# Kernel optimization log

Measured on AMD Instinct MI355X. Metric: run time of the kernel, lower is better.

The kernel has to match this reference:

```python
import jax, jax.numpy as jnp
import numpy as np

N_NODES = 100000
N_EDGES = 1600000
N_FEAT = 128
HIDDEN = 128
N_GRAPHS = 64
N_CLASSES = 10
BN_EPS = 1e-5


def setup_inputs() -> dict:
    key = jax.random.key(0)
    ks = jax.random.split(key, 24)
    glorot = lambda k, o, i: jax.random.normal(k, (o, i), jnp.float32) * (1.0 / np.sqrt(i))
    inp = {
        'x': jax.random.normal(ks[0], (N_NODES, N_FEAT), jnp.float32),
        'edge_index': jax.random.randint(ks[1], (2, N_EDGES), 0, N_NODES, jnp.int64),
        'batch': jnp.sort(jax.random.randint(ks[2], (N_NODES,), 0, N_GRAPHS, jnp.int64)),
        # GCNConv(128 -> 128)
        'gcn_w': glorot(ks[3], HIDDEN, N_FEAT),
        'gcn_b': jnp.zeros((HIDDEN,), jnp.float32),
        # SAGEConv layers 1, 2: lin_l (aggregated, with bias) + lin_r (root, no bias)
        'sage1_wl': glorot(ks[4], HIDDEN, HIDDEN),
        'sage1_bl': jnp.zeros((HIDDEN,), jnp.float32),
        'sage1_wr': glorot(ks[5], HIDDEN, HIDDEN),
        'sage2_wl': glorot(ks[6], HIDDEN, HIDDEN),
        'sage2_bl': jnp.zeros((HIDDEN,), jnp.float32),
        'sage2_wr': glorot(ks[7], HIDDEN, HIDDEN),
        # ClassifierBase: 128 -> 200 -> 100 -> 50 -> 10
        'clf_w0': glorot(ks[8], 200, HIDDEN), 'clf_b0': jnp.zeros((200,), jnp.float32),
        'clf_w1': glorot(ks[9], 100, 200), 'clf_b1': jnp.zeros((100,), jnp.float32),
        'clf_w2': glorot(ks[10], 50, 100), 'clf_b2': jnp.zeros((50,), jnp.float32),
        'clf_w3': glorot(ks[11], N_CLASSES, 50), 'clf_b3': jnp.zeros((N_CLASSES,), jnp.float32),
        # BatchNorm1d (eval mode, running_mean=0, running_var=1)
        'bn0_g': jnp.ones((200,), jnp.float32), 'bn0_b': jnp.zeros((200,), jnp.float32),
        'bn1_g': jnp.ones((100,), jnp.float32), 'bn1_b': jnp.zeros((100,), jnp.float32),
        'bn2_g': jnp.ones((50,), jnp.float32), 'bn2_b': jnp.zeros((50,), jnp.float32),
    }
    return inp


def _gcn_conv(x, src, dst, W, b):
    # PyG GCNConv: add self loops, symmetric deg^{-1/2} normalization
    xw = x @ W.T                                                  # [N, H]
    ones = jnp.ones(src.shape[0], xw.dtype)
    deg = jax.ops.segment_sum(ones, dst, num_segments=N_NODES) + 1.0  # self loops
    dinv = jax.lax.rsqrt(deg)
    norm = dinv[src] * dinv[dst]                                  # [E]
    out = jax.ops.segment_sum(xw[src] * norm[:, None], dst, num_segments=N_NODES)
    out = out + xw * (dinv * dinv)[:, None]                       # self-loop term deg^{-1}
    return out + b


def _sage_conv(x, src, dst, Wl, bl, Wr):
    # PyG SAGEConv (mean aggr): lin_l(mean_{j->i} x_j) + lin_r(x_i)
    ones = jnp.ones(src.shape[0], x.dtype)
    cnt = jax.ops.segment_sum(ones, dst, num_segments=N_NODES)
    agg = jax.ops.segment_sum(x[src], dst, num_segments=N_NODES)
    agg = agg / jnp.maximum(cnt, 1.0)[:, None]
    return agg @ Wl.T + bl + x @ Wr.T


def _bn_eval(h, g, b):
    # eval-mode BatchNorm1d with running_mean=0, running_var=1
    return h * (g / np.sqrt(1.0 + BN_EPS)) + b


def reference(x, edge_index, batch, gcn_w, gcn_b,
              sage1_wl, sage1_bl, sage1_wr, sage2_wl, sage2_bl, sage2_wr,
              clf_w0, clf_b0, clf_w1, clf_b1, clf_w2, clf_b2, clf_w3, clf_b3,
              bn0_g, bn0_b, bn1_g, bn1_b, bn2_g, bn2_b):
    src, dst = edge_index[0], edge_index[1]
    h = _gcn_conv(x, src, dst, gcn_w, gcn_b)          # act_func is None -> no activation
    h = _sage_conv(h, src, dst, sage1_wl, sage1_bl, sage1_wr)
    h = _sage_conv(h, src, dst, sage2_wl, sage2_bl, sage2_wr)
    # global mean pool over graphs
    gcnt = jax.ops.segment_sum(jnp.ones(h.shape[0], h.dtype), batch, num_segments=N_GRAPHS)
    g = jax.ops.segment_sum(h, batch, num_segments=N_GRAPHS) / jnp.maximum(gcnt, 1.0)[:, None]
    # ClassifierBase (eval: dropout inactive), tanh activation
    g = jnp.tanh(_bn_eval(g @ clf_w0.T + clf_b0, bn0_g, bn0_b))
    g = jnp.tanh(_bn_eval(g @ clf_w1.T + clf_b1, bn1_g, bn1_b))
    g = jnp.tanh(_bn_eval(g @ clf_w2.T + clf_b2, bn2_g, bn2_b))
    logits = g @ clf_w3.T + clf_b3
    return jax.nn.softmax(logits, axis=1)             # [B, n_classes]
```

## Files before the change

### kernel.cpp

```cpp
#include <hip/hip_runtime.h>

#define N_NODES 100000
#define N_EDGES 1600000
#define NGRAPH 64
#define NBIN 391
#define EPB 2560
#define NBLK 625
#define CAPB 6144
#define CAPP 7168
#define PSPLIT 8

typedef short s8v __attribute__((ext_vector_type(8)));
typedef float f4v __attribute__((ext_vector_type(4)));
typedef float f2v __attribute__((ext_vector_type(2)));

__device__ __forceinline__ float bflo(unsigned u) { return __uint_as_float(u << 16); }
__device__ __forceinline__ float bfhi(unsigned u) { return __uint_as_float(u & 0xffff0000u); }
__device__ __forceinline__ unsigned short f2bf(float f) {
    unsigned u = __float_as_uint(f);
    u += 0x7fffu + ((u >> 16) & 1u);
    return (unsigned short)(u >> 16);
}
__device__ __forceinline__ float bf2f(unsigned short h) { return __uint_as_float(((unsigned)h) << 16); }
__device__ __forceinline__ unsigned pk(float lo, float hi) {
    return (unsigned)f2bf(lo) | ((unsigned)f2bf(hi) << 16);
}
__device__ __forceinline__ float ldv(const void* p, int i, int f32) {
    return f32 ? ((const float*)p)[i] : bf2f(((const unsigned short*)p)[i]);
}
__device__ __forceinline__ f2v up2(unsigned u) {
    f2v t; t.x = bflo(u); t.y = bfhi(u); return t;
}

__global__ __launch_bounds__(256) void k_setup(const unsigned short* __restrict__ x,
                                               const int* __restrict__ ei,
                                               const int* __restrict__ batch,
                                               int* __restrict__ flags,
                                               int* __restrict__ binCur,
                                               int* __restrict__ gstart,
                                               float* __restrict__ pbuf,
                                               const void* b0, const void* bn0g, const void* bn0b,
                                               const void* b1, const void* bn1g, const void* bn1b,
                                               const void* b2, const void* bn2g, const void* bn2b,
                                               const void* b3) {
    __shared__ int cnt[3];
    int tid = threadIdx.x;
    if (tid < 3) cnt[tid] = 0;
    __syncthreads();
    unsigned short h = x[tid * 37];
    int e = (h >> 7) & 0xFF;
    if (e >= 100 && e <= 150) atomicAdd(&cnt[0], 1);
    if (ei[2 * (tid * 5000) + 1] == 0) atomicAdd(&cnt[1], 1);
    if (batch[2 * (tid * 193) + 1] == 0) atomicAdd(&cnt[2], 1);
    __syncthreads();
    int f = (cnt[0] == 256) ? 0 : 1;
    int b64 = (cnt[2] == 256) ? 1 : 0;
    if (tid == 0) {
        flags[0] = f;
        flags[1] = (cnt[1] == 256) ? 1 : 0;
        flags[2] = b64;
    }
    for (int i = tid; i < NBIN; i += 256) binCur[i] = i * CAPB;
    if (tid <= NGRAPH) {
        int g = tid, lo = 0, hi = N_NODES;
        while (lo < hi) {
            int mid = (lo + hi) >> 1;
            int v = b64 ? batch[2 * mid] : batch[mid];
            if (v < g) lo = mid + 1;
            else hi = mid;
        }
        gstart[g] = lo;
    }
    const float invs = rsqrtf(1.0f + 1e-5f);
    if (tid < 200) {
        float a = ldv(bn0g, tid, f) * invs;
        pbuf[tid] = a;
        pbuf[200 + tid] = ldv(b0, tid, f) * a + ldv(bn0b, tid, f);
    }
    if (tid < 100) {
        float a = ldv(bn1g, tid, f) * invs;
        pbuf[400 + tid] = a;
        pbuf[500 + tid] = ldv(b1, tid, f) * a + ldv(bn1b, tid, f);
    }
    if (tid < 50) {
        float a = ldv(bn2g, tid, f) * invs;
        pbuf[600 + tid] = a;
        pbuf[650 + tid] = ldv(b2, tid, f) * a + ldv(bn2b, tid, f);
    }
    if (tid < 10) pbuf[700 + tid] = ldv(b3, tid, f);
}

__global__ __launch_bounds__(256) void k_binfill(const int* __restrict__ ei,
                                                 int* __restrict__ binCur,
                                                 unsigned* __restrict__ staging,
                                                 const int* __restrict__ flags) {
    __shared__ int cnt[NBIN];
    __shared__ int lofs[NBIN];
    __shared__ int curL[NBIN];
    __shared__ int basg[NBIN];
    __shared__ int sA[512], sB[512];
    __shared__ int sbuf[EPB];
    __shared__ int dbuf[EPB];
    __shared__ unsigned ebuf[EPB];
    __shared__ unsigned short bbuf[EPB];
    int tid = threadIdx.x;
    int i64 = flags[1];
    int base = blockIdx.x * EPB;
    for (int i = tid; i < NBIN; i += 256) cnt[i] = 0;
    __syncthreads();
    #pragma unroll
    for (int k = 0; k < EPB / 512; ++k) {
        int e = base + k * 512 + tid * 2;
        int s0, s1, d0, d1;
        if (i64) {
            uint4 vs = *(const uint4*)(ei + 2 * (size_t)e);
            uint4 vd = *(const uint4*)(ei + 2 * (size_t)(N_EDGES + e));
            s0 = (int)vs.x; s1 = (int)vs.z;
            d0 = (int)vd.x; d1 = (int)vd.z;
        } else {
            int2 vs = *(const int2*)(ei + (size_t)e);
            int2 vd = *(const int2*)(ei + (size_t)N_EDGES + e);
            s0 = vs.x; s1 = vs.y;
            d0 = vd.x; d1 = vd.y;
        }
        int l = k * 512 + tid * 2;
        sbuf[l] = s0; sbuf[l + 1] = s1;
        dbuf[l] = d0; dbuf[l + 1] = d1;
        if ((unsigned)d0 < N_NODES) atomicAdd(&cnt[d0 >> 8], 1);
        if ((unsigned)d1 < N_NODES) atomicAdd(&cnt[d1 >> 8], 1);
    }
    __syncthreads();
    for (int k = tid; k < 512; k += 256) sA[k] = (k < NBIN) ? cnt[k] : 0;
    __syncthreads();
    int* src = sA;
    int* dst = sB;
    for (int off = 1; off < 512; off <<= 1) {
        for (int k = tid; k < 512; k += 256)
            dst[k] = src[k] + ((k >= off) ? src[k - off] : 0);
        __syncthreads();
        int* t = src; src = dst; dst = t;
    }
    int totE = src[NBIN - 1];
    for (int i = tid; i < NBIN; i += 256) {
        int excl = src[i] - cnt[i];
        lofs[i] = excl;
        curL[i] = excl;
        basg[i] = cnt[i] ? atomicAdd(&binCur[i], cnt[i]) : 0;
    }
    __syncthreads();
    #pragma unroll
    for (int k = 0; k < EPB / 256; ++k) {
        int l = k * 256 + tid;
        int d = dbuf[l];
        int s = sbuf[l];
        if ((unsigned)d < N_NODES) {
            s = min(max(s, 0), N_NODES - 1);
            int p = atomicAdd(&curL[d >> 8], 1);
            ebuf[p] = ((unsigned)(d & 255) << 20) | (unsigned)s;
            bbuf[p] = (unsigned short)(d >> 8);
        }
    }
    __syncthreads();
    for (int i = tid; i < totE; i += 256) {
        int bb = bbuf[i];
        int p = basg[bb] + (i - lofs[bb]);
        if (p < (bb + 1) * CAPB) staging[p] = ebuf[i];
    }
}

__global__ __launch_bounds__(256) void k_csr(const unsigned* __restrict__ staging,
                                             const int* __restrict__ binCur,
                                             int* __restrict__ rsA, int* __restrict__ reA,
                                             float* __restrict__ dinv,
                                             int* __restrict__ colidx) {
    __shared__ int deg[256];
    __shared__ int s[256];
    __shared__ int cur[256];
    __shared__ int colbuf[CAPP];
    int b = blockIdx.x, tid = threadIdx.x;
    int n0 = b << 8;
    int nend = min(256, N_NODES - n0);
    int runStart = b * CAPB;
    int outStart = b * CAPP;
    int runLen = min(binCur[b] - runStart, CAPB);
    deg[tid] = 0;
    for (int i = tid; i < CAPP; i += 256) colbuf[i] = N_NODES;
    __syncthreads();
    for (int i = tid; i < runLen; i += 256)
        atomicAdd(&deg[staging[runStart + i] >> 20], 1);
    __syncthreads();
    int myDeg = deg[tid];
    int pdeg = (myDeg + 15) & ~15;
    s[tid] = pdeg;
    __syncthreads();
    for (int off = 1; off < 256; off <<= 1) {
        int x2 = (tid >= off) ? s[tid - off] : 0;
        __syncthreads();
        s[tid] += x2;
        __syncthreads();
    }
    int incl = s[tid];
    int lrs = incl - pdeg;
    if (tid < nend) {
        rsA[n0 + tid] = outStart + lrs;
        reA[n0 + tid] = outStart + lrs + myDeg;
        dinv[n0 + tid] = rsqrtf((float)myDeg + 1.0f);
    }
    cur[tid] = lrs;
    __syncthreads();
    for (int i = tid; i < runLen; i += 256) {
        unsigned e = staging[runStart + i];
        int p = atomicAdd(&cur[e >> 20], 1);
        if (p < CAPP) colbuf[p] = (int)(e & 0xFFFFF);
    }
    __syncthreads();
    int ptot = min(s[255], CAPP);
    for (int i = tid; i < ptot; i += 256) colidx[outStart + i] = colbuf[i];
}

__global__ __launch_bounds__(256) void k_prescale(const void* __restrict__ src,
                                                  const float* __restrict__ dinv,
                                                  unsigned* __restrict__ out,
                                                  unsigned* __restrict__ padA,
                                                  const int* __restrict__ flags) {
    int id = blockIdx.x * 256 + threadIdx.x;
    if (id >= (N_NODES + 1) * 64) return;
    int node = id >> 6;
    if (node == N_NODES) {
        out[id] = 0u;
        padA[id] = 0u;
        return;
    }
    float di = dinv[node];
    float lo, hi;
    if (flags[0]) {
        float2 u = ((const float2*)src)[id];
        lo = u.x; hi = u.y;
    } else {
        unsigned u = ((const unsigned*)src)[id];
        lo = bflo(u); hi = bfhi(u);
    }
    out[id] = pk(di * lo, di * hi);
}

__global__ __launch_bounds__(256) void k_agg(const uint4* __restrict__ xs,
                                             const int* __restrict__ rsA,
                                             const int* __restrict__ reA,
                                             const float* __restrict__ dinv,
                                             unsigned* __restrict__ out, int mode,
                                             const int* __restrict__ col) {
    int lane = threadIdx.x & 63;
    int node = blockIdx.x * 4 + (threadIdx.x >> 6);
    int glane = lane & 15, grp = lane >> 4;
    int rs = rsA[node], re = reA[node];
    int deg = re - rs;
    int pend = rs + ((deg + 15) & ~15);
    f2v a0 = {0.f, 0.f}, a1 = {0.f, 0.f}, a2 = {0.f, 0.f}, a3 = {0.f, 0.f};
    uint4 selfu = make_uint4(0u, 0u, 0u, 0u);
    if (mode == 0) selfu = xs[(unsigned)node * 16u + glane];

    for (int base = rs; base < pend; base += 16) {
        int4 c = *(const int4*)(col + base + grp * 4);
        uint4 u0 = xs[(unsigned)c.x * 16u + glane];
        uint4 u1 = xs[(unsigned)c.y * 16u + glane];
        uint4 u2 = xs[(unsigned)c.z * 16u + glane];
        uint4 u3 = xs[(unsigned)c.w * 16u + glane];
        a0 += up2(u0.x); a1 += up2(u0.y); a2 += up2(u0.z); a3 += up2(u0.w);
        a0 += up2(u1.x); a1 += up2(u1.y); a2 += up2(u1.z); a3 += up2(u1.w);
        a0 += up2(u2.x); a1 += up2(u2.y); a2 += up2(u2.z); a3 += up2(u2.w);
        a0 += up2(u3.x); a1 += up2(u3.y); a2 += up2(u3.z); a3 += up2(u3.w);
    }
    float r[8] = {a0.x, a0.y, a1.x, a1.y, a2.x, a2.y, a3.x, a3.y};
    #pragma unroll
    for (int i = 0; i < 8; ++i) {
        float v = r[i];
        v += __shfl_xor(v, 16, 64);
        v += __shfl_xor(v, 32, 64);
        r[i] = v;
    }
    if (mode == 0) {
        float di = dinv[node];
        r[0] = di * (r[0] + bflo(selfu.x)); r[1] = di * (r[1] + bfhi(selfu.x));
        r[2] = di * (r[2] + bflo(selfu.y)); r[3] = di * (r[3] + bfhi(selfu.y));
        r[4] = di * (r[4] + bflo(selfu.z)); r[5] = di * (r[5] + bfhi(selfu.z));
        r[6] = di * (r[6] + bflo(selfu.w)); r[7] = di * (r[7] + bfhi(selfu.w));
    } else {
        float s = 1.0f / fmaxf((float)deg, 1.0f);
        #pragma unroll
        for (int i = 0; i < 8; ++i) r[i] *= s;
    }
    if (grp == 0) {
        uint4 o;
        o.x = pk(r[0], r[1]); o.y = pk(r[2], r[3]);
        o.z = pk(r[4], r[5]); o.w = pk(r[6], r[7]);
        *(uint4*)(out + (size_t)node * 64 + glane * 4) = o;
    }
}

template <int DUAL>
__global__ __launch_bounds__(256) void k_gemm(const unsigned short* A0,
                                              const void* __restrict__ W0,
                                              const unsigned short* __restrict__ A1,
                                              const void* __restrict__ W1,
                                              const void* __restrict__ bias,
                                              unsigned short* out,
                                              const int* __restrict__ flags) {
    __shared__ __align__(16) unsigned short As[64][136];
    __shared__ __align__(16) unsigned short Ws[128][136];
    int f32 = flags[0];
    int tid = threadIdx.x;
    int lane = tid & 63;
    int rowbase = blockIdx.x * 64;
    int lr = lane & 15, q = lane >> 4;
    int m0 = (tid >> 6) * 16;

    f4v acc[8];
    #pragma unroll
    for (int t = 0; t < 8; ++t) acc[t] = (f4v){0.f, 0.f, 0.f, 0.f};

    #pragma unroll
    for (int p = 0; p < (DUAL ? 2 : 1); ++p) {
        const unsigned short* Ap = p ? A1 : A0;
        const void* Wp = p ? W1 : W0;
        if (p) __syncthreads();
        #pragma unroll
        for (int it = 0; it < 4; ++it) {
            int chunk = tid + it * 256;
            int r = chunk >> 4, c8 = (chunk & 15) * 8;
            int grow = rowbase + r;
            uint4 v = make_uint4(0u, 0u, 0u, 0u);
            if (grow < N_NODES) v = *(const uint4*)(Ap + (size_t)grow * 128 + c8);
            *(uint4*)&As[r][c8] = v;
        }
        if (!f32) {
            const unsigned short* Wf = (const unsigned short*)Wp;
            #pragma unroll
            for (int it = 0; it < 8; ++it) {
                int chunk = tid + it * 256;
                int r = chunk >> 4, c8 = (chunk & 15) * 8;
                *(uint4*)&Ws[r][c8] = *(const uint4*)(Wf + r * 128 + c8);
            }
        } else {
            const float* Wf = (const float*)Wp;
            #pragma unroll
            for (int it = 0; it < 16; ++it) {
                int chunk = tid + it * 256;
                int r = chunk >> 5, c4 = (chunk & 31) * 4;
                float4 v = *(const float4*)(Wf + r * 128 + c4);
                unsigned lo = (unsigned)f2bf(v.x) | ((unsigned)f2bf(v.y) << 16);
                unsigned hi = (unsigned)f2bf(v.z) | ((unsigned)f2bf(v.w) << 16);
                *(uint2*)&Ws[r][c4] = make_uint2(lo, hi);
            }
        }
        __syncthreads();
        #pragma unroll
        for (int k = 0; k < 4; ++k) {
            s8v a = *(const s8v*)&As[m0 + lr][k * 32 + q * 8];
            #pragma unroll
            for (int t = 0; t < 8; ++t) {
                s8v b = *(const s8v*)&Ws[t * 16 + lr][k * 32 + q * 8];
                acc[t] = __builtin_amdgcn_mfma_f32_16x16x32_bf16(a, b, acc[t], 0, 0, 0);
            }
        }
    }
    #pragma unroll
    for (int t = 0; t < 8; ++t) {
        int o = t * 16 + lr;
        float bv = ldv(bias, o, f32);
        #pragma unroll
        for (int j = 0; j < 4; ++j) {
            int m = rowbase + m0 + q * 4 + j;
            if (m < N_NODES) out[(size_t)m * 128 + o] = f2bf(acc[t][j] + bv);
        }
    }
}

__global__ __launch_bounds__(256) void k_pool2(const unsigned* __restrict__ h,
                                               const int* __restrict__ gstart,
                                               float* __restrict__ ppool) {
    __shared__ float part[4][128];
    int g = blockIdx.x / PSPLIT, sl = blockIdx.x % PSPLIT;
    int wave = threadIdx.x >> 6, lane = threadIdx.x & 63;
    int s0 = gstart[g], s1 = gstart[g + 1];
    int n = s1 - s0;
    int chunk = (n + PSPLIT - 1) / PSPLIT;
    int r0 = s0 + sl * chunk;
    int r1 = min(r0 + chunk, s1);
    float a0 = 0.f, a1 = 0.f;
    for (int r = r0 + wave; r < r1; r += 4) {
        unsigned u = h[(size_t)r * 64 + lane];
        a0 += bflo(u);
        a1 += bfhi(u);
    }
    part[wave][2 * lane] = a0;
    part[wave][2 * lane + 1] = a1;
    __syncthreads();
    int t = threadIdx.x;
    if (t < 128) {
        float s = part[0][t] + part[1][t] + part[2][t] + part[3][t];
        ppool[(size_t)blockIdx.x * 128 + t] = s;
    }
}

__global__ void k_cvt_w(const void* w0, const void* w1, const void* w2, const void* w3,
                        float* __restrict__ wbuf, const int* __restrict__ flags) {
    int f = flags[0];
    int i = blockIdx.x * 256 + threadIdx.x;
    if (i < 25600) wbuf[i] = ldv(w0, i, f);
    else if (i < 45600) wbuf[i] = ldv(w1, i - 25600, f);
    else if (i < 50600) wbuf[i] = ldv(w2, i - 45600, f);
    else if (i < 51100) wbuf[i] = ldv(w3, i - 50600, f);
}

__global__ __launch_bounds__(256) void k_clf(const float* __restrict__ ppool,
                                             const int* __restrict__ gstart,
                                             const float* __restrict__ wbuf,
                                             const float* __restrict__ pbuf,
                                             void* outv, const int* __restrict__ flags) {
    __shared__ float gin[128];
    __shared__ float ha[200];
    __shared__ float hb[100];
    int b = blockIdx.x, t = threadIdx.x;
    if (t < 128) {
        float s = 0.f;
        #pragma unroll
        for (int k = 0; k < PSPLIT; ++k) s += ppool[(size_t)(b * PSPLIT + k) * 128 + t];
        int cnt = gstart[b + 1] - gstart[b];
        gin[t] = s / fmaxf((float)cnt, 1.0f);
    }
    __syncthreads();
    if (t < 200) {
        const float4* wr = (const float4*)(wbuf + t * 128);
        float s = 0.f;
        #pragma unroll
        for (int k = 0; k < 32; ++k) {
            float4 v = wr[k];
            s += v.x * gin[4 * k] + v.y * gin[4 * k + 1] + v.z * gin[4 * k + 2] + v.w * gin[4 * k + 3];
        }
        ha[t] = tanhf(s * pbuf[t] + pbuf[200 + t]);
    }
    __syncthreads();
    if (t < 100) {
        const float4* wr = (const float4*)(wbuf + 25600 + t * 200);
        float s = 0.f;
        #pragma unroll
        for (int k = 0; k < 50; ++k) {
            float4 v = wr[k];
            s += v.x * ha[4 * k] + v.y * ha[4 * k + 1] + v.z * ha[4 * k + 2] + v.w * ha[4 * k + 3];
        }
        hb[t] = tanhf(s * pbuf[400 + t] + pbuf[500 + t]);
    }
    __syncthreads();
    if (t < 50) {
        const float4* wr = (const float4*)(wbuf + 45600 + t * 100);
        float s = 0.f;
        #pragma unroll
        for (int k = 0; k < 25; ++k) {
            float4 v = wr[k];
            s += v.x * hb[4 * k] + v.y * hb[4 * k + 1] + v.z * hb[4 * k + 2] + v.w * hb[4 * k + 3];
        }
        gin[t] = tanhf(s * pbuf[600 + t] + pbuf[650 + t]);
    }
    __syncthreads();
    if (t == 0) {
        int f = flags[0];
        float lg[10];
        float mx = -1e30f;
        #pragma unroll
        for (int c = 0; c < 10; ++c) {
            const float* wr = wbuf + 50600 + c * 50;
            float s = 0.f;
            for (int k = 0; k < 50; ++k) s += wr[k] * gin[k];
            s += pbuf[700 + c];
            lg[c] = s;
            mx = fmaxf(mx, s);
        }
        float sum = 0.f;
        #pragma unroll
        for (int c = 0; c < 10; ++c) {
            lg[c] = __expf(lg[c] - mx);
            sum += lg[c];
        }
        float inv = 1.0f / sum;
        #pragma unroll
        for (int c = 0; c < 10; ++c) {
            float v = lg[c] * inv;
            if (f) ((float*)outv)[b * 10 + c] = v;
            else ((unsigned short*)outv)[b * 10 + c] = f2bf(v);
        }
    }
}

extern "C" void kernel_launch(void* const* d_in, const int* in_sizes, int n_in,
                              void* d_out, int out_size, void* d_ws, size_t ws_size,
                              hipStream_t stream) {
    const unsigned short* x16 = (const unsigned short*)d_in[0];
    const int* ei = (const int*)d_in[1];
    const int* batch = (const int*)d_in[2];

    char* ws = (char*)d_ws;
    size_t off = 0;
    auto alloc = [&](size_t bytes) {
        size_t r = off;
        off = (off + bytes + 255) & ~(size_t)255;
        return r;
    };
    int* flags = (int*)(ws + alloc(256));
    int* rsA = (int*)(ws + alloc((size_t)N_NODES * 4));
    int* reA = (int*)(ws + alloc((size_t)N_NODES * 4));
    int* colidx = (int*)(ws + alloc((size_t)NBIN * CAPP * 4));
    float* dinv = (float*)(ws + alloc((size_t)N_NODES * 4));
    int* binCur = (int*)(ws + alloc(NBIN * 4));
    int* gstart = (int*)(ws + alloc((NGRAPH + 1) * 4));
    float* pbuf = (float*)(ws + alloc(710 * 4));
    float* ppool = (float*)(ws + alloc((size_t)NGRAPH * PSPLIT * 128 * 4));
    float* wbuf = (float*)(ws + alloc(51100 * 4));
    unsigned short* bufA = (unsigned short*)(ws + alloc((size_t)(N_NODES + 1) * 128 * 2));
    unsigned short* bufB = (unsigned short*)(ws + alloc((size_t)(N_NODES + 1) * 128 * 2));
    unsigned* staging = (unsigned*)bufA;

    k_setup<<<1, 256, 0, stream>>>(x16, ei, batch, flags, binCur, gstart, pbuf,
                                   d_in[12], d_in[19], d_in[20],
                                   d_in[14], d_in[21], d_in[22],
                                   d_in[16], d_in[23], d_in[24], d_in[18]);
    k_cvt_w<<<200, 256, 0, stream>>>(d_in[11], d_in[13], d_in[15], d_in[17], wbuf, flags);

    k_binfill<<<NBLK, 256, 0, stream>>>(ei, binCur, staging, flags);
    k_csr<<<NBIN, 256, 0, stream>>>(staging, binCur, rsA, reA, dinv, colidx);

    k_prescale<<<((N_NODES + 1) * 64 + 255) / 256, 256, 0, stream>>>(
        (const void*)x16, dinv, (unsigned*)bufB, (unsigned*)bufA, flags);
    k_agg<<<N_NODES / 4, 256, 0, stream>>>((const uint4*)bufB, rsA, reA, dinv,
                                           (unsigned*)bufA, 0, colidx);
    k_gemm<0><<<(N_NODES + 63) / 64, 256, 0, stream>>>(bufA, d_in[3], nullptr, nullptr, d_in[4],
                                                       bufA, flags);
    k_agg<<<N_NODES / 4, 256, 0, stream>>>((const uint4*)bufA, rsA, reA, dinv,
                                           (unsigned*)bufB, 1, colidx);
    k_gemm<1><<<(N_NODES + 63) / 64, 256, 0, stream>>>(bufB, d_in[5], bufA, d_in[7], d_in[6],
                                                       bufB, flags);
    k_agg<<<N_NODES / 4, 256, 0, stream>>>((const uint4*)bufB, rsA, reA, dinv,
                                           (unsigned*)bufA, 1, colidx);
    k_gemm<1><<<(N_NODES + 63) / 64, 256, 0, stream>>>(bufA, d_in[8], bufB, d_in[10], d_in[9],
                                                       bufA, flags);
    k_pool2<<<NGRAPH * PSPLIT, 256, 0, stream>>>((const unsigned*)bufA, gstart, ppool);
    k_clf<<<NGRAPH, 256, 0, stream>>>(ppool, gstart, wbuf, pbuf, d_out, flags);
}
```

Before: 500.2 us.

## Fold GCN prescale into aggregation, merge setup kernels, enlarge GEMM tiles

New measurement: 473.2 us. -5.4%, faster.

```diff
diff --git a/kernel.cpp b/kernel.cpp
--- a/kernel.cpp
+++ b/kernel.cpp
@@ -39,28 +39,39 @@
                                                int* __restrict__ binCur,
                                                int* __restrict__ gstart,
                                                float* __restrict__ pbuf,
+                                               float* __restrict__ wbuf,
+                                               const void* w0, const void* w1,
+                                               const void* w2, const void* w3,
                                                const void* b0, const void* bn0g, const void* bn0b,
                                                const void* b1, const void* bn1g, const void* bn1b,
                                                const void* b2, const void* bn2g, const void* bn2b,
                                                const void* b3) {
     __shared__ int cnt[3];
-    int tid = threadIdx.x;
+    int tid = threadIdx.x, bid = blockIdx.x;
     if (tid < 3) cnt[tid] = 0;
     __syncthreads();
     unsigned short h = x[tid * 37];
     int e = (h >> 7) & 0xFF;
     if (e >= 100 && e <= 150) atomicAdd(&cnt[0], 1);
-    if (ei[2 * (tid * 5000) + 1] == 0) atomicAdd(&cnt[1], 1);
-    if (batch[2 * (tid * 193) + 1] == 0) atomicAdd(&cnt[2], 1);
+    if (bid == 0) {
+        if (ei[2 * (tid * 5000) + 1] == 0) atomicAdd(&cnt[1], 1);
+        if (batch[2 * (tid * 193) + 1] == 0) atomicAdd(&cnt[2], 1);
+    }
     __syncthreads();
     int f = (cnt[0] == 256) ? 0 : 1;
+    int i = bid * 256 + tid;
+    if (i < 25600) wbuf[i] = ldv(w0, i, f);
+    else if (i < 45600) wbuf[i] = ldv(w1, i - 25600, f);
+    else if (i < 50600) wbuf[i] = ldv(w2, i - 45600, f);
+    else if (i < 51100) wbuf[i] = ldv(w3, i - 50600, f);
+    if (bid != 0) return;
     int b64 = (cnt[2] == 256) ? 1 : 0;
     if (tid == 0) {
         flags[0] = f;
         flags[1] = (cnt[1] == 256) ? 1 : 0;
         flags[2] = b64;
     }
-    for (int i = tid; i < NBIN; i += 256) binCur[i] = i * CAPB;
+    for (int k = tid; k < NBIN; k += 256) binCur[k] = k * CAPB;
     if (tid <= NGRAPH) {
         int g = tid, lo = 0, hi = N_NODES;
         while (lo < hi) {
@@ -170,9 +181,11 @@
 
 __global__ __launch_bounds__(256) void k_csr(const unsigned* __restrict__ staging,
                                              const int* __restrict__ binCur,
-                                             int* __restrict__ rsA, int* __restrict__ reA,
+                                             int2* __restrict__ rse,
                                              float* __restrict__ dinv,
-                                             int* __restrict__ colidx) {
+                                             int* __restrict__ colidx,
+                                             unsigned* __restrict__ padA,
+                                             unsigned* __restrict__ padB) {
     __shared__ int deg[256];
     __shared__ int s[256];
     __shared__ int cur[256];
@@ -202,8 +215,7 @@
     int incl = s[tid];
     int lrs = incl - pdeg;
     if (tid < nend) {
-        rsA[n0 + tid] = outStart + lrs;
-        reA[n0 + tid] = outStart + lrs + myDeg;
+        rse[n0 + tid] = make_int2(outStart + lrs, outStart + lrs + myDeg);
         dinv[n0 + tid] = rsqrtf((float)myDeg + 1.0f);
     }
     cur[tid] = lrs;
@@ -216,59 +228,71 @@
     __syncthreads();
     int ptot = min(s[255], CAPP);
     for (int i = tid; i < ptot; i += 256) colidx[outStart + i] = colbuf[i];
-}
-
-__global__ __launch_bounds__(256) void k_prescale(const void* __restrict__ src,
-                                                  const float* __restrict__ dinv,
-                                                  unsigned* __restrict__ out,
-                                                  unsigned* __restrict__ padA,
-                                                  const int* __restrict__ flags) {
+    if (b == 0) {
+        if (tid < 64) {
+            padA[(size_t)N_NODES * 64 + tid] = 0u;
+            padB[(size_t)N_NODES * 64 + tid] = 0u;
+        }
+        if (tid == 0) dinv[N_NODES] = 0.f;
+    }
+}
+
+__global__ __launch_bounds__(256) void k_cvtx(const void* __restrict__ src,
+                                              unsigned* __restrict__ out,
+                                              const int* __restrict__ flags) {
+    if (!flags[0]) return;
     int id = blockIdx.x * 256 + threadIdx.x;
-    if (id >= (N_NODES + 1) * 64) return;
-    int node = id >> 6;
-    if (node == N_NODES) {
-        out[id] = 0u;
-        padA[id] = 0u;
-        return;
-    }
-    float di = dinv[node];
-    float lo, hi;
-    if (flags[0]) {
-        float2 u = ((const float2*)src)[id];
-        lo = u.x; hi = u.y;
-    } else {
-        unsigned u = ((const unsigned*)src)[id];
-        lo = bflo(u); hi = bfhi(u);
-    }
-    out[id] = pk(di * lo, di * hi);
-}
-
-__global__ __launch_bounds__(256) void k_agg(const uint4* __restrict__ xs,
-                                             const int* __restrict__ rsA,
-                                             const int* __restrict__ reA,
+    if (id >= N_NODES * 64) return;
+    float2 u = ((const float2*)src)[id];
+    out[id] = pk(u.x, u.y);
+}
+
+template <int MODE>
+__global__ __launch_bounds__(256) void k_agg(const uint4* __restrict__ xsA,
+                                             const uint4* __restrict__ xsB,
+                                             const int2* __restrict__ rse,
                                              const float* __restrict__ dinv,
-                                             unsigned* __restrict__ out, int mode,
-                                             const int* __restrict__ col) {
+                                             unsigned* __restrict__ out,
+                                             const int* __restrict__ col,
+                                             const int* __restrict__ flags) {
     int lane = threadIdx.x & 63;
     int node = blockIdx.x * 4 + (threadIdx.x >> 6);
     int glane = lane & 15, grp = lane >> 4;
-    int rs = rsA[node], re = reA[node];
-    int deg = re - rs;
+    const uint4* xs = (MODE == 0) ? (flags[0] ? xsB : xsA) : xsA;
+    int2 rr = rse[node];
+    int rs = rr.x, deg = rr.y - rr.x;
     int pend = rs + ((deg + 15) & ~15);
     f2v a0 = {0.f, 0.f}, a1 = {0.f, 0.f}, a2 = {0.f, 0.f}, a3 = {0.f, 0.f};
     uint4 selfu = make_uint4(0u, 0u, 0u, 0u);
-    if (mode == 0) selfu = xs[(unsigned)node * 16u + glane];
+    float di = 0.f;
+    if (MODE == 0) {
+        selfu = xs[(unsigned)node * 16u + glane];
+        di = dinv[node];
+    }
 
     for (int base = rs; base < pend; base += 16) {
         int4 c = *(const int4*)(col + base + grp * 4);
+        float dv0, dv1, dv2, dv3;
+        if (MODE == 0) {
+            dv0 = dinv[c.x]; dv1 = dinv[c.y]; dv2 = dinv[c.z]; dv3 = dinv[c.w];
+            c.x = min(c.x, N_NODES - 1); c.y = min(c.y, N_NODES - 1);
+            c.z = min(c.z, N_NODES - 1); c.w = min(c.w, N_NODES - 1);
+        }
         uint4 u0 = xs[(unsigned)c.x * 16u + glane];
         uint4 u1 = xs[(unsigned)c.y * 16u + glane];
         uint4 u2 = xs[(unsigned)c.z * 16u + glane];
         uint4 u3 = xs[(unsigned)c.w * 16u + glane];
-        a0 += up2(u0.x); a1 += up2(u0.y); a2 += up2(u0.z); a3 += up2(u0.w);
-        a0 += up2(u1.x); a1 += up2(u1.y); a2 += up2(u1.z); a3 += up2(u1.w);
-        a0 += up2(u2.x); a1 += up2(u2.y); a2 += up2(u2.z); a3 += up2(u2.w);
-        a0 += up2(u3.x); a1 += up2(u3.y); a2 += up2(u3.z); a3 += up2(u3.w);
+        if (MODE == 0) {
+            a0 += dv0 * up2(u0.x); a1 += dv0 * up2(u0.y); a2 += dv0 * up2(u0.z); a3 += dv0 * up2(u0.w);
+            a0 += dv1 * up2(u1.x); a1 += dv1 * up2(u1.y); a2 += dv1 * up2(u1.z); a3 += dv1 * up2(u1.w);
+            a0 += dv2 * up2(u2.x); a1 += dv2 * up2(u2.y); a2 += dv2 * up2(u2.z); a3 += dv2 * up2(u2.w);
+            a0 += dv3 * up2(u3.x); a1 += dv3 * up2(u3.y); a2 += dv3 * up2(u3.z); a3 += dv3 * up2(u3.w);
+        } else {
+            a0 += up2(u0.x); a1 += up2(u0.y); a2 += up2(u0.z); a3 += up2(u0.w);
+            a0 += up2(u1.x); a1 += up2(u1.y); a2 += up2(u1.z); a3 += up2(u1.w);
+            a0 += up2(u2.x); a1 += up2(u2.y); a2 += up2(u2.z); a3 += up2(u2.w);
+            a0 += up2(u3.x); a1 += up2(u3.y); a2 += up2(u3.z); a3 += up2(u3.w);
+        }
     }
     float r[8] = {a0.x, a0.y, a1.x, a1.y, a2.x, a2.y, a3.x, a3.y};
     #pragma unroll
@@ -278,12 +302,12 @@
         v += __shfl_xor(v, 32, 64);
         r[i] = v;
     }
-    if (mode == 0) {
-        float di = dinv[node];
-        r[0] = di * (r[0] + bflo(selfu.x)); r[1] = di * (r[1] + bfhi(selfu.x));
-        r[2] = di * (r[2] + bflo(selfu.y)); r[3] = di * (r[3] + bfhi(selfu.y));
-        r[4] = di * (r[4] + bflo(selfu.z)); r[5] = di * (r[5] + bfhi(selfu.z));
-        r[6] = di * (r[6] + bflo(selfu.w)); r[7] = di * (r[7] + bfhi(selfu.w));
+    if (MODE == 0) {
+        float d2 = di * di;
+        r[0] = di * r[0] + d2 * bflo(selfu.x); r[1] = di * r[1] + d2 * bfhi(selfu.x);
+        r[2] = di * r[2] + d2 * bflo(selfu.y); r[3] = di * r[3] + d2 * bfhi(selfu.y);
+        r[4] = di * r[4] + d2 * bflo(selfu.z); r[5] = di * r[5] + d2 * bfhi(selfu.z);
+        r[6] = di * r[6] + d2 * bflo(selfu.w); r[7] = di * r[7] + d2 * bfhi(selfu.w);
     } else {
         float s = 1.0f / fmaxf((float)deg, 1.0f);
         #pragma unroll
@@ -298,19 +322,19 @@
 }
 
 template <int DUAL>
-__global__ __launch_bounds__(256) void k_gemm(const unsigned short* A0,
+__global__ __launch_bounds__(512) void k_gemm(const unsigned short* A0,
                                               const void* __restrict__ W0,
                                               const unsigned short* __restrict__ A1,
                                               const void* __restrict__ W1,
                                               const void* __restrict__ bias,
                                               unsigned short* out,
                                               const int* __restrict__ flags) {
-    __shared__ __align__(16) unsigned short As[64][136];
+    __shared__ __align__(16) unsigned short As[128][136];
     __shared__ __align__(16) unsigned short Ws[128][136];
     int f32 = flags[0];
     int tid = threadIdx.x;
     int lane = tid & 63;
-    int rowbase = blockIdx.x * 64;
+    int rowbase = blockIdx.x * 128;
     int lr = lane & 15, q = lane >> 4;
     int m0 = (tid >> 6) * 16;
 
@@ -325,7 +349,7 @@
         if (p) __syncthreads();
         #pragma unroll
         for (int it = 0; it < 4; ++it) {
-            int chunk = tid + it * 256;
+            int chunk = tid + it * 512;
             int r = chunk >> 4, c8 = (chunk & 15) * 8;
             int grow = rowbase + r;
             uint4 v = make_uint4(0u, 0u, 0u, 0u);
@@ -335,16 +359,16 @@
         if (!f32) {
             const unsigned short* Wf = (const unsigned short*)Wp;
             #pragma unroll
-            for (int it = 0; it < 8; ++it) {
-                int chunk = tid + it * 256;
+            for (int it = 0; it < 4; ++it) {
+                int chunk = tid + it * 512;
                 int r = chunk >> 4, c8 = (chunk & 15) * 8;
                 *(uint4*)&Ws[r][c8] = *(const uint4*)(Wf + r * 128 + c8);
             }
         } else {
             const float* Wf = (const float*)Wp;
             #pragma unroll
-            for (int it = 0; it < 16; ++it) {
-                int chunk = tid + it * 256;
+            for (int it = 0; it < 8; ++it) {
+                int chunk = tid + it * 512;
                 int r = chunk >> 5, c4 = (chunk & 31) * 4;
                 float4 v = *(const float4*)(Wf + r * 128 + c4);
                 unsigned lo = (unsigned)f2bf(v.x) | ((unsigned)f2bf(v.y) << 16);
@@ -402,16 +426,6 @@
     }
 }
 
-__global__ void k_cvt_w(const void* w0, const void* w1, const void* w2, const void* w3,
-                        float* __restrict__ wbuf, const int* __restrict__ flags) {
-    int f = flags[0];
-    int i = blockIdx.x * 256 + threadIdx.x;
-    if (i < 25600) wbuf[i] = ldv(w0, i, f);
-    else if (i < 45600) wbuf[i] = ldv(w1, i - 25600, f);
-    else if (i < 50600) wbuf[i] = ldv(w2, i - 45600, f);
-    else if (i < 51100) wbuf[i] = ldv(w3, i - 50600, f);
-}
-
 __global__ __launch_bounds__(256) void k_clf(const float* __restrict__ ppool,
                                              const int* __restrict__ gstart,
                                              const float* __restrict__ wbuf,
@@ -506,10 +520,9 @@
         return r;
     };
     int* flags = (int*)(ws + alloc(256));
-    int* rsA = (int*)(ws + alloc((size_t)N_NODES * 4));
-    int* reA = (int*)(ws + alloc((size_t)N_NODES * 4));
+    int2* rse = (int2*)(ws + alloc((size_t)N_NODES * 8));
     int* colidx = (int*)(ws + alloc((size_t)NBIN * CAPP * 4));
-    float* dinv = (float*)(ws + alloc((size_t)N_NODES * 4));
+    float* dinv = (float*)(ws + alloc((size_t)(N_NODES + 1) * 4));
     int* binCur = (int*)(ws + alloc(NBIN * 4));
     int* gstart = (int*)(ws + alloc((NGRAPH + 1) * 4));
     float* pbuf = (float*)(ws + alloc(710 * 4));
@@ -519,29 +532,30 @@
     unsigned short* bufB = (unsigned short*)(ws + alloc((size_t)(N_NODES + 1) * 128 * 2));
     unsigned* staging = (unsigned*)bufA;
 
-    k_setup<<<1, 256, 0, stream>>>(x16, ei, batch, flags, binCur, gstart, pbuf,
-                                   d_in[12], d_in[19], d_in[20],
-                                   d_in[14], d_in[21], d_in[22],
-                                   d_in[16], d_in[23], d_in[24], d_in[18]);
-    k_cvt_w<<<200, 256, 0, stream>>>(d_in[11], d_in[13], d_in[15], d_in[17], wbuf, flags);
+    k_setup<<<200, 256, 0, stream>>>(x16, ei, batch, flags, binCur, gstart, pbuf, wbuf,
+                                     d_in[11], d_in[13], d_in[15], d_in[17],
+                                     d_in[12], d_in[19], d_in[20],
+                                     d_in[14], d_in[21], d_in[22],
+                                     d_in[16], d_in[23], d_in[24], d_in[18]);
 
     k_binfill<<<NBLK, 256, 0, stream>>>(ei, binCur, staging, flags);
-    k_csr<<<NBIN, 256, 0, stream>>>(staging, binCur, rsA, reA, dinv, colidx);
-
-    k_prescale<<<((N_NODES + 1) * 64 + 255) / 256, 256, 0, stream>>>(
-        (const void*)x16, dinv, (unsigned*)bufB, (unsigned*)bufA, flags);
-    k_agg<<<N_NODES / 4, 256, 0, stream>>>((const uint4*)bufB, rsA, reA, dinv,
-                                           (unsigned*)bufA, 0, colidx);
-    k_gemm<0><<<(N_NODES + 63) / 64, 256, 0, stream>>>(bufA, d_in[3], nullptr, nullptr, d_in[4],
-                                                       bufA, flags);
-    k_agg<<<N_NODES / 4, 256, 0, stream>>>((const uint4*)bufA, rsA, reA, dinv,
-                                           (unsigned*)bufB, 1, colidx);
-    k_gemm<1><<<(N_NODES + 63) / 64, 256, 0, stream>>>(bufB, d_in[5], bufA, d_in[7], d_in[6],
-                                                       bufB, flags);
-    k_agg<<<N_NODES / 4, 256, 0, stream>>>((const uint4*)bufB, rsA, reA, dinv,
-                                           (unsigned*)bufA, 1, colidx);
-    k_gemm<1><<<(N_NODES + 63) / 64, 256, 0, stream>>>(bufA, d_in[8], bufB, d_in[10], d_in[9],
-                                                       bufA, flags);
+    k_csr<<<NBIN, 256, 0, stream>>>(staging, binCur, rse, dinv, colidx,
+                                    (unsigned*)bufA, (unsigned*)bufB);
+    k_cvtx<<<(N_NODES * 64 + 255) / 256, 256, 0, stream>>>((const void*)x16,
+                                                           (unsigned*)bufB, flags);
+
+    k_agg<0><<<N_NODES / 4, 256, 0, stream>>>((const uint4*)x16, (const uint4*)bufB,
+                                              rse, dinv, (unsigned*)bufA, colidx, flags);
+    k_gemm<0><<<(N_NODES + 127) / 128, 512, 0, stream>>>(bufA, d_in[3], nullptr, nullptr,
+                                                         d_in[4], bufA, flags);
+    k_agg<1><<<N_NODES / 4, 256, 0, stream>>>((const uint4*)bufA, (const uint4*)bufA,
+                                              rse, dinv, (unsigned*)bufB, colidx, flags);
+    k_gemm<1><<<(N_NODES + 127) / 128, 512, 0, stream>>>(bufB, d_in[5], bufA, d_in[7],
+                                                         d_in[6], bufB, flags);
+    k_agg<1><<<N_NODES / 4, 256, 0, stream>>>((const uint4*)bufB, (const uint4*)bufB,
+                                              rse, dinv, (unsigned*)bufA, colidx, flags);
+    k_gemm<1><<<(N_NODES + 127) / 128, 512, 0, stream>>>(bufA, d_in[8], bufB, d_in[10],
+                                                         d_in[9], bufA, flags);
     k_pool2<<<NGRAPH * PSPLIT, 256, 0, stream>>>((const unsigned*)bufA, gstart, ppool);
     k_clf<<<NGRAPH, 256, 0, stream>>>(ppool, gstart, wbuf, pbuf, d_out, flags);
 }
```
